# Performance work log

Measured on AMD Instinct MI355X. Metric: run time of the kernel, lower is better.

The kernel has to match this reference:

```python
import jax, jax.numpy as jnp
import numpy as np

PRE_NMS_TOPK = 6000
POST_NMS_TOPK = 1000
NMS_THRESH = 0.7
MIN_SIZE = 16.0
NEG = -1e9  # stand-in for -inf that is safe under autodiff


def setup_inputs() -> dict:
    key = jax.random.key(0)
    k1, k2, k3, k4, k5, k6, k7, k8 = jax.random.split(key, 8)
    B, A = 8, 200000
    N = B * A
    # realistic anchors: centers within a ~1333x800 canvas, sizes 16..256
    cx = jax.random.uniform(k1, (N,), minval=0.0, maxval=1200.0)
    cy = jax.random.uniform(k2, (N,), minval=0.0, maxval=800.0)
    w = jax.random.uniform(k3, (N,), minval=16.0, maxval=256.0)
    h = jax.random.uniform(k4, (N,), minval=16.0, maxval=256.0)
    anchors = jnp.stack([cx - 0.5 * w, cy - 0.5 * h, cx + 0.5 * w, cy + 0.5 * h], axis=1)
    batch_indices = jnp.sort(jax.random.randint(k5, (N,), 0, B)).astype(jnp.int32)
    image_sizes = jax.random.randint(k6, (B, 2), 600, 1334).astype(jnp.int32)  # (H, W)
    objectness_logits = jax.random.normal(k7, (N, 1), dtype=jnp.float32)
    bbox_deltas = jax.random.normal(k8, (N, 4), dtype=jnp.float32) * 0.2
    return {
        'anchors': anchors,
        'batch_indices': batch_indices,
        'image_sizes': image_sizes,
        'objectness_logits': objectness_logits,
        'bbox_deltas': bbox_deltas,
    }


def _nms_one(bx, sc):
    """Greedy NMS on [K,4] boxes / [K] scores; returns POST_NMS_TOPK (idx, ok)."""
    K = bx.shape[0]
    areas = (bx[:, 2] - bx[:, 0]) * (bx[:, 3] - bx[:, 1])
    ar = jnp.arange(K)

    def step(sup, _):
        s = jnp.where(sup, NEG, sc)
        j = jnp.argmax(s)
        ok = s[j] > 0.5 * NEG
        b = bx[j]
        ix1 = jnp.maximum(b[0], bx[:, 0])
        iy1 = jnp.maximum(b[1], bx[:, 1])
        ix2 = jnp.minimum(b[2], bx[:, 2])
        iy2 = jnp.minimum(b[3], bx[:, 3])
        inter = jnp.maximum(ix2 - ix1, 0.0) * jnp.maximum(iy2 - iy1, 0.0)
        iou = inter / (areas + areas[j] - inter + 1e-9)
        sup = sup | (iou > NMS_THRESH) | (ar == j)
        return sup, (j, ok)

    sup0 = sc <= 0.5 * NEG  # padded / invalid entries start suppressed
    _, (idx, ok) = jax.lax.scan(step, sup0, None, length=POST_NMS_TOPK)
    return idx, ok


def reference(anchors, batch_indices, image_sizes, objectness_logits, bbox_deltas):
    B = image_sizes.shape[0]
    N = anchors.shape[0]
    sizes = image_sizes[batch_indices].astype(jnp.float32)  # [N,2] (H,W) per anchor

    # --- box decode ---
    a_w = anchors[:, 2] - anchors[:, 0]
    a_h = anchors[:, 3] - anchors[:, 1]
    a_x = anchors[:, 0] + 0.5 * a_w
    a_y = anchors[:, 1] + 0.5 * a_h
    t_x, t_y = bbox_deltas[:, 0], bbox_deltas[:, 1]
    t_w, t_h = bbox_deltas[:, 2], bbox_deltas[:, 3]
    p_x = a_x + t_x * a_w
    p_y = a_y + t_y * a_h
    p_w = a_w * jnp.exp(jnp.clip(t_w, -10.0, 10.0))
    p_h = a_h * jnp.exp(jnp.clip(t_h, -10.0, 10.0))
    x1 = p_x - 0.5 * p_w
    y1 = p_y - 0.5 * p_h
    x2 = p_x + 0.5 * p_w
    y2 = p_y + 0.5 * p_h

    # --- clip to image ---
    H, W = sizes[:, 0], sizes[:, 1]
    x1 = jnp.clip(x1, 0.0, W - 1.0)
    y1 = jnp.clip(y1, 0.0, H - 1.0)
    x2 = jnp.clip(x2, 0.0, W - 1.0)
    y2 = jnp.clip(y2, 0.0, H - 1.0)
    boxes = jnp.stack([x1, y1, x2, y2], axis=1)  # [N,4]

    # --- min-size filter (as score masking) ---
    valid = ((x2 - x1) >= MIN_SIZE) & ((y2 - y1) >= MIN_SIZE)
    fg = jax.nn.sigmoid(objectness_logits[:, 0])

    # --- per-image top-k over masked scores ---
    img_mask = batch_indices[None, :] == jnp.arange(B, dtype=batch_indices.dtype)[:, None]  # [B,N]
    scores = jnp.where(img_mask & valid[None, :], fg[None, :], NEG)  # [B,N]
    top_scores, top_idx = jax.lax.top_k(scores, PRE_NMS_TOPK)  # [B,PRE]
    top_boxes = boxes[top_idx]  # [B,PRE,4]

    # --- NMS per image ---
    keep_idx, keep_ok = jax.vmap(_nms_one)(top_boxes, top_scores)  # [B,POST]

    sel = jnp.take_along_axis(top_idx, keep_idx, axis=1)  # global anchor indices [B,POST]
    okf = keep_ok[..., None].astype(boxes.dtype)
    props = jnp.take_along_axis(top_boxes, keep_idx[..., None], axis=1) * okf  # [B,POST,4]
    obj = objectness_logits[sel] * okf  # [B,POST,1]
    deltas_out = bbox_deltas[sel] * okf  # [B,POST,4]
    bidx = jnp.where(keep_ok, jnp.arange(B, dtype=jnp.int32)[:, None], -1)  # [B,POST]

    return (props.reshape(-1, 4), bidx.reshape(-1), obj.reshape(-1, 1),
            deltas_out.reshape(-1, 4), keep_ok.reshape(-1))
```

## Files before the change

### kernel.cpp

```cpp
#include <hip/hip_runtime.h>
#include <stdint.h>

#define PRE_K   6000
#define POST_K  1000
#define CAP     8192
#define BINS    1024
#define ROWS    6016
#define CH      94
#define JSPLIT  8
#define NEGF    -1000000000.0f
#define IOU_EPS 16.0f
#define KREG    12


__device__ __forceinline__ uint32_t orderf(float f) {
  uint32_t u = __float_as_uint(f);
  return (u & 0x80000000u) ? ~u : (u | 0x80000000u);
}

__device__ __forceinline__ int score_bin(float sc) {
  int bin = (int)floorf((sc + 12.0f) * ((float)BINS / 24.0f));
  return bin < 0 ? 0 : (bin > BINS - 1 ? BINS - 1 : bin);
}

__device__ __forceinline__ int bin_slot(int bin) {
  return ((bin & 15) << 6) | (bin >> 4);
}

__device__ __forceinline__ void decode_box(
    const float* __restrict__ anchors, const float* __restrict__ deltas,
    const int* __restrict__ isz, int n, int b,
    double& x1, double& y1, double& x2, double& y2, bool& valid) {
  double ax1 = (double)anchors[4 * n + 0], ay1 = (double)anchors[4 * n + 1];
  double ax2 = (double)anchors[4 * n + 2], ay2 = (double)anchors[4 * n + 3];
  double aw = ax2 - ax1, ah = ay2 - ay1;
  double acx = ax1 + 0.5 * aw, acy = ay1 + 0.5 * ah;
  double tx = (double)deltas[4 * n + 0], ty = (double)deltas[4 * n + 1];
  double tw = (double)deltas[4 * n + 2], th = (double)deltas[4 * n + 3];
  tw = tw < -10.0 ? -10.0 : (tw > 10.0 ? 10.0 : tw);
  th = th < -10.0 ? -10.0 : (th > 10.0 ? 10.0 : th);
  double px = acx + tx * aw, py = acy + ty * ah;
  double pw = aw * exp(tw), ph = ah * exp(th);
  double H = (double)isz[2 * b + 0], W = (double)isz[2 * b + 1];
  double wm = W - 1.0, hm = H - 1.0;
  x1 = px - 0.5 * pw; y1 = py - 0.5 * ph;
  x2 = px + 0.5 * pw; y2 = py + 0.5 * ph;
  x1 = fmin(fmax(x1, 0.0), wm); x2 = fmin(fmax(x2, 0.0), wm);
  y1 = fmin(fmax(y1, 0.0), hm); y2 = fmin(fmax(y2, 0.0), hm);
  valid = (x2 - x1 >= 16.0) && (y2 - y1 >= 16.0);
}

__device__ __forceinline__ bool iou_exact(const double* __restrict__ tbox,
                                          const double* __restrict__ tarea,
                                          size_t ri, size_t ci) {
  const double* pr = &tbox[ri * 4];
  const double* pc = &tbox[ci * 4];
  double w = fmin(pr[2], pc[2]) - fmax(pr[0], pc[0]); w = w > 0.0 ? w : 0.0;
  double h = fmin(pr[3], pc[3]) - fmax(pr[1], pc[1]); h = h > 0.0 ? h : 0.0;
  double it = w * h;
  return it > 0.7 * (tarea[ri] + tarea[ci] - it + 1e-9);
}


__global__ void __launch_bounds__(256) k_score(const float* __restrict__ anchors,
                                               const int* __restrict__ bix,
                                               const int* __restrict__ isz,
                                               const float* __restrict__ logits,
                                               const float* __restrict__ deltas,
                                               float* __restrict__ scores,
                                               uint32_t* __restrict__ hist, int N) {
  const int SPAN = 4096;
  int start = blockIdx.x * SPAN;
  int end = start + SPAN < N ? start + SPAN : N;
  __shared__ uint32_t lh[2][BINS];
  for (int i = threadIdx.x; i < 2 * BINS; i += 256) ((uint32_t*)lh)[i] = 0u;
  __shared__ int s_b0, s_b1;
  if (threadIdx.x == 0) { s_b0 = bix[start]; s_b1 = bix[end - 1]; }
  __syncthreads();
  int b0 = s_b0, b1 = s_b1;

  for (int n = start + (int)threadIdx.x; n < end; n += 256) {
    int b = bix[n];
    double x1, y1, x2, y2; bool valid;
    decode_box(anchors, deltas, isz, n, b, x1, y1, x2, y2, valid);
    float sc = valid ? logits[n] : NEGF;
    scores[n] = sc;
    if (valid) {
      int bin = score_bin(sc);
      if (b == b0)      atomicAdd(&lh[0][bin], 1u);
      else if (b == b1) atomicAdd(&lh[1][bin], 1u);
      else              atomicAdd(&hist[b * BINS + bin_slot(bin)], 1u);
    }
  }
  __syncthreads();
  for (int bin = threadIdx.x; bin < BINS; bin += 256) {
    uint32_t c0 = lh[0][bin];
    if (c0) atomicAdd(&hist[b0 * BINS + bin_slot(bin)], c0);
    if (b1 != b0) {
      uint32_t c1 = lh[1][bin];
      if (c1) atomicAdd(&hist[b1 * BINS + bin_slot(bin)], c1);
    }
  }
}

__global__ void __launch_bounds__(1024) k_compact(const float* __restrict__ scores,
                                                  const int* __restrict__ bix,
                                                  const uint32_t* __restrict__ hist,
                                                  uint32_t* __restrict__ cnt,
                                                  uint64_t* __restrict__ cand, int N) {
  const int SPAN = 8192;
  int start = blockIdx.x * SPAN;
  int end = start + SPAN < N ? start + SPAN : N;
  int t = threadIdx.x;
  __shared__ int s_b0, s_b1;
  __shared__ uint32_t sh[BINS];
  __shared__ int s_bs;
  __shared__ uint32_t lcnt[8], lbase[8];
  if (t == 0) { s_b0 = bix[start]; s_b1 = bix[end - 1]; }
  if (t < 8) lcnt[t] = 0u;
  __syncthreads();
  int b0 = s_b0, b1 = s_b1;

  uint32_t bs0 = 0, bs1 = 0;
  for (int pass = 0; pass < 2; pass++) {
    int b = pass == 0 ? b0 : b1;
    if (pass == 1 && b1 == b0) { bs1 = bs0; break; }
    if (t < BINS) sh[t] = hist[b * BINS + bin_slot(t)];
    if (t == 0) s_bs = 0;
    __syncthreads();
    for (int off = 1; off < BINS; off <<= 1) {
      uint32_t v = (t < BINS && t + off < BINS) ? sh[t + off] : 0u;
      __syncthreads();
      if (t < BINS) sh[t] += v;
      __syncthreads();
    }
    if (t < BINS && sh[t] >= PRE_K) atomicMax(&s_bs, t);
    __syncthreads();
    if (pass == 0) bs0 = (uint32_t)s_bs; else bs1 = (uint32_t)s_bs;
    __syncthreads();
  }

  bool     predv[8];
  uint64_t keyv[8];
  uint32_t lposv[8];
  int      bv[8];
  int nt = 0;
  for (int base = start; base < end; base += 1024, nt++) {
    int n = base + t;
    bool pred = false; int b = 0; uint64_t key = 0ull; uint32_t lp = 0u;
    if (n < end) {
      float sc = scores[n];
      if (sc > 0.5f * NEGF) {
        b = bix[n];
        uint32_t bs = (b == b0) ? bs0 : bs1;
        if ((uint32_t)score_bin(sc) >= bs) {
          pred = true;
          key = ((uint64_t)orderf(sc) << 32) | (uint64_t)(uint32_t)(~(uint32_t)n);
          lp = atomicAdd(&lcnt[b], 1u);
        }
      }
    }
    predv[nt] = pred; keyv[nt] = key; lposv[nt] = lp; bv[nt] = b;
  }
  __syncthreads();
  if (t < 8) {
    uint32_t c = lcnt[t];
    lbase[t] = c ? atomicAdd(&cnt[t], c) : 0u;
  }
  __syncthreads();
  for (int k = 0; k < nt; k++) {
    if (predv[k]) {
      uint32_t pos = lbase[bv[k]] + lposv[k];
      if (pos < CAP) cand[(size_t)bv[k] * CAP + pos] = keyv[k];
    }
  }
}

__global__ void __launch_bounds__(256) k_rank(const uint64_t* __restrict__ cand,
                                              const uint32_t* __restrict__ cnt,
                                              uint32_t* __restrict__ prank) {
  int blk = blockIdx.x;
  int js = blk % JSPLIT;
  int ic = (blk / JSPLIT) % 32;
  int b  = blk / (JSPLIT * 32);
  int t = threadIdx.x;
  int C = (int)min(cnt[b], (uint32_t)CAP);
  if (ic * 256 >= C) return;
  const uint64_t* g = cand + (size_t)b * CAP;
  int i = ic * 256 + t;
  uint64_t ki = (i < C) ? g[i] : 0ull;

  int q = (C + JSPLIT - 1) / JSPLIT;
  int j0 = js * q;
  int j1 = j0 + q < C ? j0 + q : C;

  __shared__ uint64_t tile[1024];
  int rank = 0;
  for (int base = j0; base < j1; base += 1024) {
#pragma unroll
    for (int u = 0; u < 4; u++) {
      int j = base + u * 256 + t;
      tile[u * 256 + t] = (j < j1) ? g[j] : 0ull;
    }
    __syncthreads();
    int lim = j1 - base < 1024 ? j1 - base : 1024;
    const ulonglong2* t2 = (const ulonglong2*)tile;
    int pairs = lim >> 1;
    int jj = 0;
    for (; jj + 4 <= pairs; jj += 4) {
      ulonglong2 v0 = t2[jj + 0], v1 = t2[jj + 1];
      ulonglong2 v2 = t2[jj + 2], v3 = t2[jj + 3];
      rank += (v0.x > ki) ? 1 : 0; rank += (v0.y > ki) ? 1 : 0;
      rank += (v1.x > ki) ? 1 : 0; rank += (v1.y > ki) ? 1 : 0;
      rank += (v2.x > ki) ? 1 : 0; rank += (v2.y > ki) ? 1 : 0;
      rank += (v3.x > ki) ? 1 : 0; rank += (v3.y > ki) ? 1 : 0;
    }
    for (; jj < pairs; jj++) {
      ulonglong2 v = t2[jj];
      rank += (v.x > ki) ? 1 : 0; rank += (v.y > ki) ? 1 : 0;
    }
    if (lim & 1) rank += (tile[lim - 1] > ki) ? 1 : 0;
    __syncthreads();
  }
  if (i < C) prank[((size_t)b * JSPLIT + js) * CAP + i] = (uint32_t)rank;
}

__global__ void __launch_bounds__(256) k_place_gather(
    const uint64_t* __restrict__ cand, const uint32_t* __restrict__ cnt,
    const uint32_t* __restrict__ prank,
    const float* __restrict__ anchors, const float* __restrict__ deltas,
    const int* __restrict__ isz,
    double* __restrict__ tbox, double* __restrict__ tarea,
    float4* __restrict__ tboxf, float* __restrict__ tareaf,
    int* __restrict__ top_n, int* __restrict__ Cnum, int B) {
  int idx = blockIdx.x * blockDim.x + threadIdx.x;
  if (idx >= B * CAP) return;
  int b = idx / CAP, i = idx % CAP;
  int C = (int)min(cnt[b], (uint32_t)CAP);
  if (i == 0) Cnum[b] = C < PRE_K ? C : PRE_K;
  if (i >= C) return;
  uint32_t rank = 0;
#pragma unroll
  for (int js = 0; js < JSPLIT; js++)
    rank += prank[((size_t)b * JSPLIT + js) * CAP + i];
  if (rank >= PRE_K) return;
  int n = (int)(~(uint32_t)(cand[idx] & 0xFFFFFFFFull));
  double x1, y1, x2, y2; bool valid;
  decode_box(anchors, deltas, isz, n, b, x1, y1, x2, y2, valid);
  size_t row = (size_t)b * ROWS + rank;
  tbox[row * 4 + 0] = x1;
  tbox[row * 4 + 1] = y1;
  tbox[row * 4 + 2] = x2;
  tbox[row * 4 + 3] = y2;
  double ar = (x2 - x1) * (y2 - y1);
  tarea[row] = ar;
  tboxf[row] = make_float4((float)x1, (float)y1, (float)x2, (float)y2);
  tareaf[row] = (float)ar;
  top_n[b * PRE_K + rank] = n;
}

__global__ void __launch_bounds__(64) k_iou_mat(const float4* __restrict__ tboxf,
                                                const float* __restrict__ tareaf,
                                                const double* __restrict__ tbox,
                                                const double* __restrict__ tarea,
                                                const int* __restrict__ Cnum,
                                                uint32_t* __restrict__ maskT) {
  int rc = blockIdx.x;
  int cc = blockIdx.y;
  int b  = blockIdx.z;
  if (rc > cc) return;
  int C = Cnum[b];
  if (cc * 64 >= C) return;
  int lane = threadIdx.x;
  size_t bb = (size_t)b * ROWS;

  float4 rb4 = tboxf[bb + (size_t)rc * 64 + lane];
  float  sra = 0.7f * tareaf[bb + (size_t)rc * 64 + lane];
  __shared__ float4 cbx[64];
  __shared__ float  csa[64];
  cbx[lane] = tboxf[bb + (size_t)cc * 64 + lane];
  csa[lane] = 0.7f * tareaf[bb + (size_t)cc * 64 + lane];
  __syncthreads();

  bool isdiag = (rc == cc);
  uint32_t res0 = 0u, res1 = 0u;

  for (int j = 0; j < 64; j++) {
    float4 c4 = cbx[j];
    float sca = csa[j];
    float iw = fminf(c4.z, rb4.z) - fmaxf(c4.x, rb4.x);
    float ih = fminf(c4.w, rb4.w) - fmaxf(c4.y, rb4.y);
    iw = fmaxf(iw, 0.0f); ih = fmaxf(ih, 0.0f);
    float inter = iw * ih;
    float diff = fmaf(1.7f, inter, -(sra + sca));
    bool gt = isdiag ? (j > lane) : true;
    bool sup = gt && (diff > IOU_EPS);
    if (gt && !sup && diff > -IOU_EPS) {
      sup = iou_exact(tbox, tarea, bb + (size_t)rc * 64 + lane,
                      bb + (size_t)cc * 64 + j);
    }
    if (sup) { if (j < 32) res0 |= 1u << j; else res1 |= 1u << (j & 31); }
  }
  uint2* seg = (uint2*)(maskT + (((size_t)b * CH + cc) * ROWS + (size_t)rc * 64) * 2);
  seg[lane] = make_uint2(res0, res1);
}

__global__ void __launch_bounds__(256) k_nms_reduce(const uint32_t* __restrict__ maskT,
                                                    const double* __restrict__ tbox,
                                                    const int* __restrict__ Cnum,
                                                    const int* __restrict__ top_n,
                                                    const float* __restrict__ logits,
                                                    const float* __restrict__ deltas,
                                                    float* __restrict__ out, int B) {
  int b = blockIdx.x, t = threadIdx.x;
  int wave = t >> 6, lane = t & 63;
  int C = Cnum[b];
  int nch = (C + 63) >> 6;
  const uint32_t* Mb = maskT + (size_t)b * CH * ROWS * 2;
  size_t bb = (size_t)b * ROWS;

  __shared__ uint32_t acc[CH][2];
  __shared__ uint16_t kept[POST_K];
  __shared__ uint16_t pend[2][64];
  __shared__ int      npend[2];
  __shared__ uint64_t s_kept;

  for (int i = t; i < CH * 2; i += 256) ((uint32_t*)acc)[i] = 0u;
  if (t < 2) npend[t] = 0;
  __syncthreads();

  uint2 dgv = make_uint2(0u, 0u), pfv = make_uint2(0u, 0u), pfv2 = make_uint2(0u, 0u);
  if (wave == 0 && nch > 0) {
    dgv = *(const uint2*)(Mb + ((size_t)0 * ROWS + lane) * 2);
    if (nch > 1) pfv  = *(const uint2*)(Mb + ((size_t)1 * ROWS + lane) * 2);
    if (nch > 2) pfv2 = *(const uint2*)(Mb + ((size_t)2 * ROWS + lane) * 2);
  }

  uint2 lz[KREG];
#pragma unroll
  for (int u = 0; u < KREG; u++) lz[u] = make_uint2(0u, 0u);
  int lz_total = 0, lz_cc0 = 0, lz_span = 1;

  int nkept = 0;
  for (int c = 0; c < nch; c++) {
    if (wave == 0) {
      int base = c << 6;
      uint64_t sup = (uint64_t)acc[c][0] | ((uint64_t)acc[c][1] << 32);
      int rem = C - base;
      if (rem < 64) sup |= ~((1ull << rem) - 1ull);
      uint64_t diag = (uint64_t)dgv.x | ((uint64_t)dgv.y << 32);
      uint64_t keptMask = 0ull;
      uint64_t alive = ~sup;
      uint64_t m = alive;
      while (m) {
        int i = __builtin_ctzll(m);
        keptMask |= 1ull << i;
        uint64_t d = (uint64_t)__shfl((long long)diag, i, 64);
        sup |= d | (1ull << i);
        m = alive & ~sup;
      }
      int allowed = POST_K - nkept;
      int pc2 = __popcll(keptMask);
      while (pc2 > allowed) {
        keptMask &= ~(1ull << (63 - __builtin_clzll(keptMask)));
        pc2--;
      }
      if (lane == 0) { s_kept = keptMask; npend[c & 1] = pc2; }
      bool mine = (keptMask >> lane) & 1ull;
      if (mine) {
        int pfx = __popcll(keptMask & ((1ull << lane) - 1ull));
        kept[nkept + pfx] = (uint16_t)(base + lane);
        pend[c & 1][pfx] = (uint16_t)(base + lane);
      }
      if (c + 1 < nch) {
        uint32_t v0 = mine ? pfv.x : 0u, v1 = mine ? pfv.y : 0u;
        uint32_t w0 = mine ? pfv2.x : 0u, w1 = mine ? pfv2.y : 0u;
#pragma unroll
        for (int off = 32; off > 0; off >>= 1) {
          v0 |= (uint32_t)__shfl_xor((int)v0, off, 64);
          v1 |= (uint32_t)__shfl_xor((int)v1, off, 64);
          w0 |= (uint32_t)__shfl_xor((int)w0, off, 64);
          w1 |= (uint32_t)__shfl_xor((int)w1, off, 64);
        }
        if (lane == 0) {
          if (v0) atomicOr(&acc[c + 1][0], v0);
          if (v1) atomicOr(&acc[c + 1][1], v1);
          if (c + 2 < nch) {
            if (w0) atomicOr(&acc[c + 2][0], w0);
            if (w1) atomicOr(&acc[c + 2][1], w1);
          }
        }
        int nb = base + 64;
        dgv = *(const uint2*)(Mb + (((size_t)(c + 1)) * ROWS + nb + lane) * 2);
        if (c + 2 < nch) pfv  = *(const uint2*)(Mb + (((size_t)(c + 2)) * ROWS + nb + lane) * 2);
        else             pfv  = make_uint2(0u, 0u);
        if (c + 3 < nch) pfv2 = *(const uint2*)(Mb + (((size_t)(c + 3)) * ROWS + nb + lane) * 2);
        else             pfv2 = make_uint2(0u, 0u);
      }
    } else {
      if (lz_total > 0) {
#pragma unroll
        for (int u = 0; u < KREG; u++) {
          int it = (t - 64) + u * 192;
          if (it < lz_total) {
            int pi = it / lz_span;
            int cc = lz_cc0 + (it - pi * lz_span);
            if (lz[u].x) atomicOr(&acc[cc][0], lz[u].x);
            if (lz[u].y) atomicOr(&acc[cc][1], lz[u].y);
          }
        }
      }
      int np = (c >= 1) ? npend[(c - 1) & 1] : 0;
      int cc0 = c + 2;
      int span = nch - cc0;
      if (np > 0 && span > 0) {
        int total = np * span;
#pragma unroll
        for (int u = 0; u < KREG; u++) {
          int it = (t - 64) + u * 192;
          uint2 v = make_uint2(0u, 0u);
          if (it < total) {
            int pi = it / span;
            int cc = cc0 + (it - pi * span);
            int row = (int)pend[(c - 1) & 1][pi];
            v = *(const uint2*)(Mb + ((size_t)cc * ROWS + row) * 2);
          }
          lz[u] = v;
        }
        for (int it = (t - 64) + KREG * 192; it < total; it += 192) {
          int pi = it / span;
          int cc = cc0 + (it - pi * span);
          int row = (int)pend[(c - 1) & 1][pi];
          uint2 v = *(const uint2*)(Mb + ((size_t)cc * ROWS + row) * 2);
          if (v.x) atomicOr(&acc[cc][0], v.x);
          if (v.y) atomicOr(&acc[cc][1], v.y);
        }
        lz_total = total < KREG * 192 ? total : KREG * 192;
        lz_cc0 = cc0; lz_span = span;
      } else {
        lz_total = 0;
      }
    }
    __syncthreads();

    int pc = __popcll(s_kept);
    nkept += pc;
    if (nkept >= POST_K) break;
  }

  __syncthreads();
  int M_out = B * POST_K;
  for (int s2 = t; s2 < POST_K; s2 += 256) {
    float p0 = 0.f, p1 = 0.f, p2 = 0.f, p3 = 0.f;
    float ob = 0.f, d0f = 0.f, d1f = 0.f, d2f = 0.f, d3f = 0.f;
    float bi = -1.0f, okv = 0.0f;
    if (s2 < nkept) {
      int j = (int)kept[s2];
      int n = top_n[b * PRE_K + j];
      const double* p = &tbox[(bb + j) * 4];
      p0 = (float)p[0]; p1 = (float)p[1]; p2 = (float)p[2]; p3 = (float)p[3];
      ob = logits[n];
      d0f = deltas[4 * n + 0]; d1f = deltas[4 * n + 1];
      d2f = deltas[4 * n + 2]; d3f = deltas[4 * n + 3];
      bi = (float)b; okv = 1.0f;
    }
    int idx = b * POST_K + s2;
    out[idx * 4 + 0] = p0;
    out[idx * 4 + 1] = p1;
    out[idx * 4 + 2] = p2;
    out[idx * 4 + 3] = p3;
    out[4 * M_out + idx] = bi;
    out[5 * M_out + idx] = ob;
    out[6 * M_out + idx * 4 + 0] = d0f;
    out[6 * M_out + idx * 4 + 1] = d1f;
    out[6 * M_out + idx * 4 + 2] = d2f;
    out[6 * M_out + idx * 4 + 3] = d3f;
    out[10 * M_out + idx] = okv;
  }
}


extern "C" void kernel_launch(void* const* d_in, const int* in_sizes, int n_in,
                              void* d_out, int out_size, void* d_ws, size_t ws_size,
                              hipStream_t stream) {
  const float* anchors = (const float*)d_in[0];
  const int*   bix     = (const int*)d_in[1];
  const int*   isz     = (const int*)d_in[2];
  const float* logits  = (const float*)d_in[3];
  const float* deltas  = (const float*)d_in[4];
  float* out = (float*)d_out;

  int N = in_sizes[1];
  int B = in_sizes[2] / 2;

  uintptr_t p = (uintptr_t)d_ws;
  double*   tbox   = (double*)p;    p += (size_t)B * ROWS * 4 * sizeof(double);
  double*   tarea  = (double*)p;    p += (size_t)B * ROWS * sizeof(double);
  uint64_t* cand   = (uint64_t*)p;  p += (size_t)B * CAP * sizeof(uint64_t);
  float*    scores = (float*)p;     p += (size_t)N * sizeof(float);
  uint32_t* hist   = (uint32_t*)p;  p += (size_t)B * BINS * sizeof(uint32_t);
  uint32_t* cnt    = (uint32_t*)p;  p += (size_t)B * sizeof(uint32_t);
  uint32_t* prank  = (uint32_t*)p;  p += (size_t)B * JSPLIT * CAP * sizeof(uint32_t);
  int*      top_n    = (int*)p;     p += (size_t)B * PRE_K * sizeof(int);
  int*      Cnum     = (int*)p;      p += (size_t)B * sizeof(int);
  p = (p + 255) & ~(uintptr_t)255;
  uint32_t* maskT    = (uint32_t*)p; p += (size_t)B * CH * ROWS * 2 * sizeof(uint32_t);
  float4*   tboxf  = (float4*)scores;
  float*    tareaf = (float*)(scores + (size_t)B * ROWS * 4);
  (void)ws_size; (void)n_in; (void)out_size;

  hipMemsetAsync(hist, 0, (size_t)(B * BINS + B) * sizeof(uint32_t), stream);
  k_score<<<(N + 4095) / 4096, 256, 0, stream>>>(anchors, bix, isz, logits, deltas,
                                                 scores, hist, N);
  k_compact<<<(N + 8191) / 8192, 1024, 0, stream>>>(scores, bix, hist, cnt, cand, N);
  k_rank<<<B * 32 * JSPLIT, 256, 0, stream>>>(cand, cnt, prank);
  k_place_gather<<<(B * CAP + 255) / 256, 256, 0, stream>>>(cand, cnt, prank,
                                                            anchors, deltas, isz,
                                                            tbox, tarea, tboxf,
                                                            tareaf, top_n, Cnum, B);
  dim3 iou_grid(CH, CH, B);
  k_iou_mat<<<iou_grid, 64, 0, stream>>>(tboxf, tareaf, tbox, tarea, Cnum, maskT);
  k_nms_reduce<<<B, 256, 0, stream>>>(maskT, tbox, Cnum, top_n, logits, deltas,
                                      out, B);
}
```

Baseline: 385.4 us.

## Fuse rank and placement kernels, restructure IoU mask layout into band and row-major

Merges the split rank kernel and the placement/gather kernel into one kernel that computes full ranks per candidate and directly decodes and places boxes, removing the partial-rank buffer and one launch. The IoU mask kernel now processes 8 column chunks per block and writes near-diagonal chunks to a compact band buffer and far chunks to a row-major buffer. The NMS reduce reads the band buffer with double-buffered prefetch and gathers far rows contiguously per row. The aim is fewer launches and more coalesced mask access, at the cost of less parallelism in ranking and more work per IoU block.

```diff
diff --git a/kernel.cpp b/kernel.cpp
--- a/kernel.cpp
+++ b/kernel.cpp
@@ -7,7 +7,7 @@
 #define BINS    1024
 #define ROWS    6016
 #define CH      94
-#define JSPLIT  8
+#define CHP     96
 #define NEGF    -1000000000.0f
 #define IOU_EPS 16.0f
 #define KREG    12
@@ -176,34 +176,33 @@
   }
 }
 
-__global__ void __launch_bounds__(256) k_rank(const uint64_t* __restrict__ cand,
-                                              const uint32_t* __restrict__ cnt,
-                                              uint32_t* __restrict__ prank) {
-  int blk = blockIdx.x;
-  int js = blk % JSPLIT;
-  int ic = (blk / JSPLIT) % 32;
-  int b  = blk / (JSPLIT * 32);
+__global__ void __launch_bounds__(256) k_rank_place(
+    const uint64_t* __restrict__ cand, const uint32_t* __restrict__ cnt,
+    const float* __restrict__ anchors, const float* __restrict__ deltas,
+    const int* __restrict__ isz,
+    double* __restrict__ tbox, double* __restrict__ tarea,
+    float4* __restrict__ tboxf, float* __restrict__ tareaf,
+    int* __restrict__ top_n, int* __restrict__ Cnum, int B) {
+  int ic = blockIdx.x & 31;
+  int b  = blockIdx.x >> 5;
   int t = threadIdx.x;
   int C = (int)min(cnt[b], (uint32_t)CAP);
+  if (ic == 0 && t == 0) Cnum[b] = C < PRE_K ? C : PRE_K;
   if (ic * 256 >= C) return;
   const uint64_t* g = cand + (size_t)b * CAP;
   int i = ic * 256 + t;
   uint64_t ki = (i < C) ? g[i] : 0ull;
 
-  int q = (C + JSPLIT - 1) / JSPLIT;
-  int j0 = js * q;
-  int j1 = j0 + q < C ? j0 + q : C;
-
   __shared__ uint64_t tile[1024];
   int rank = 0;
-  for (int base = j0; base < j1; base += 1024) {
+  for (int base = 0; base < C; base += 1024) {
 #pragma unroll
     for (int u = 0; u < 4; u++) {
       int j = base + u * 256 + t;
-      tile[u * 256 + t] = (j < j1) ? g[j] : 0ull;
-    }
-    __syncthreads();
-    int lim = j1 - base < 1024 ? j1 - base : 1024;
+      tile[u * 256 + t] = (j < C) ? g[j] : 0ull;
+    }
+    __syncthreads();
+    int lim = C - base < 1024 ? C - base : 1024;
     const ulonglong2* t2 = (const ulonglong2*)tile;
     int pairs = lim >> 1;
     int jj = 0;
@@ -222,29 +221,9 @@
     if (lim & 1) rank += (tile[lim - 1] > ki) ? 1 : 0;
     __syncthreads();
   }
-  if (i < C) prank[((size_t)b * JSPLIT + js) * CAP + i] = (uint32_t)rank;
-}
-
-__global__ void __launch_bounds__(256) k_place_gather(
-    const uint64_t* __restrict__ cand, const uint32_t* __restrict__ cnt,
-    const uint32_t* __restrict__ prank,
-    const float* __restrict__ anchors, const float* __restrict__ deltas,
-    const int* __restrict__ isz,
-    double* __restrict__ tbox, double* __restrict__ tarea,
-    float4* __restrict__ tboxf, float* __restrict__ tareaf,
-    int* __restrict__ top_n, int* __restrict__ Cnum, int B) {
-  int idx = blockIdx.x * blockDim.x + threadIdx.x;
-  if (idx >= B * CAP) return;
-  int b = idx / CAP, i = idx % CAP;
-  int C = (int)min(cnt[b], (uint32_t)CAP);
-  if (i == 0) Cnum[b] = C < PRE_K ? C : PRE_K;
-  if (i >= C) return;
-  uint32_t rank = 0;
-#pragma unroll
-  for (int js = 0; js < JSPLIT; js++)
-    rank += prank[((size_t)b * JSPLIT + js) * CAP + i];
-  if (rank >= PRE_K) return;
-  int n = (int)(~(uint32_t)(cand[idx] & 0xFFFFFFFFull));
+  if (i >= C || rank >= PRE_K) return;
+
+  int n = (int)(~(uint32_t)(ki & 0xFFFFFFFFull));
   double x1, y1, x2, y2; bool valid;
   decode_box(anchors, deltas, isz, n, b, x1, y1, x2, y2, valid);
   size_t row = (size_t)b * ROWS + rank;
@@ -264,13 +243,17 @@
                                                 const double* __restrict__ tbox,
                                                 const double* __restrict__ tarea,
                                                 const int* __restrict__ Cnum,
-                                                uint32_t* __restrict__ maskT) {
-  int rc = blockIdx.x;
-  int cc = blockIdx.y;
+                                                uint32_t* __restrict__ maskB,
+                                                uint32_t* __restrict__ maskR) {
+  int g  = blockIdx.x;
+  int rc = blockIdx.y;
   int b  = blockIdx.z;
-  if (rc > cc) return;
   int C = Cnum[b];
-  if (cc * 64 >= C) return;
+  int nch = (C + 63) >> 6;
+  if (rc >= nch) return;
+  int cc_lo = g << 3;
+  int cc_hi = (cc_lo + 8 < nch) ? cc_lo + 8 : nch;
+  if (cc_lo >= nch || cc_hi <= rc) return;
   int lane = threadIdx.x;
   size_t bb = (size_t)b * ROWS;
 
@@ -278,34 +261,59 @@
   float  sra = 0.7f * tareaf[bb + (size_t)rc * 64 + lane];
   __shared__ float4 cbx[64];
   __shared__ float  csa[64];
-  cbx[lane] = tboxf[bb + (size_t)cc * 64 + lane];
-  csa[lane] = 0.7f * tareaf[bb + (size_t)cc * 64 + lane];
-  __syncthreads();
-
-  bool isdiag = (rc == cc);
-  uint32_t res0 = 0u, res1 = 0u;
-
-  for (int j = 0; j < 64; j++) {
-    float4 c4 = cbx[j];
-    float sca = csa[j];
-    float iw = fminf(c4.z, rb4.z) - fmaxf(c4.x, rb4.x);
-    float ih = fminf(c4.w, rb4.w) - fmaxf(c4.y, rb4.y);
-    iw = fmaxf(iw, 0.0f); ih = fmaxf(ih, 0.0f);
-    float inter = iw * ih;
-    float diff = fmaf(1.7f, inter, -(sra + sca));
-    bool gt = isdiag ? (j > lane) : true;
-    bool sup = gt && (diff > IOU_EPS);
-    if (gt && !sup && diff > -IOU_EPS) {
-      sup = iou_exact(tbox, tarea, bb + (size_t)rc * 64 + lane,
-                      bb + (size_t)cc * 64 + j);
-    }
-    if (sup) { if (j < 32) res0 |= 1u << j; else res1 |= 1u << (j & 31); }
-  }
-  uint2* seg = (uint2*)(maskT + (((size_t)b * CH + cc) * ROWS + (size_t)rc * 64) * 2);
-  seg[lane] = make_uint2(res0, res1);
-}
-
-__global__ void __launch_bounds__(256) k_nms_reduce(const uint32_t* __restrict__ maskT,
+
+  uint2 fr[8];
+#pragma unroll
+  for (int u = 0; u < 8; u++) fr[u] = make_uint2(0u, 0u);
+  bool any_far = false;
+
+#pragma unroll
+  for (int u = 0; u < 8; u++) {
+    int cc = cc_lo + u;
+    if (cc < rc || cc >= cc_hi) continue;
+    __syncthreads();
+    cbx[lane] = tboxf[bb + (size_t)cc * 64 + lane];
+    csa[lane] = 0.7f * tareaf[bb + (size_t)cc * 64 + lane];
+    __syncthreads();
+    int d = cc - rc;
+    bool isdiag = (d == 0);
+    uint32_t r0 = 0u, r1 = 0u;
+    for (int j = 0; j < 64; j++) {
+      float4 c4 = cbx[j];
+      float sca = csa[j];
+      float iw = fminf(c4.z, rb4.z) - fmaxf(c4.x, rb4.x);
+      float ih = fminf(c4.w, rb4.w) - fmaxf(c4.y, rb4.y);
+      iw = fmaxf(iw, 0.0f); ih = fmaxf(ih, 0.0f);
+      float inter = iw * ih;
+      float diff = fmaf(1.7f, inter, -(sra + sca));
+      bool gt = isdiag ? (j > lane) : true;
+      bool sup = gt && (diff > IOU_EPS);
+      if (gt && !sup && diff > -IOU_EPS) {
+        sup = iou_exact(tbox, tarea, bb + (size_t)rc * 64 + lane,
+                        bb + (size_t)cc * 64 + j);
+      }
+      if (sup) { if (j < 32) r0 |= 1u << j; else r1 |= 1u << (j & 31); }
+    }
+    if (d <= 2) {
+      uint2* bp = (uint2*)maskB + (((size_t)b * CH + rc) * 3 + d) * 64;
+      bp[lane] = make_uint2(r0, r1);
+    } else {
+      fr[u] = make_uint2(r0, r1);
+      any_far = true;
+    }
+  }
+  if (any_far) {
+    size_t base = (bb + (size_t)rc * 64 + lane) * CHP + cc_lo;
+    uint4* dst = (uint4*)(maskR + base * 2);
+    dst[0] = make_uint4(fr[0].x, fr[0].y, fr[1].x, fr[1].y);
+    dst[1] = make_uint4(fr[2].x, fr[2].y, fr[3].x, fr[3].y);
+    dst[2] = make_uint4(fr[4].x, fr[4].y, fr[5].x, fr[5].y);
+    dst[3] = make_uint4(fr[6].x, fr[6].y, fr[7].x, fr[7].y);
+  }
+}
+
+__global__ void __launch_bounds__(256) k_nms_reduce(const uint32_t* __restrict__ maskB,
+                                                    const uint32_t* __restrict__ maskR,
                                                     const double* __restrict__ tbox,
                                                     const int* __restrict__ Cnum,
                                                     const int* __restrict__ top_n,
@@ -316,7 +324,8 @@
   int wave = t >> 6, lane = t & 63;
   int C = Cnum[b];
   int nch = (C + 63) >> 6;
-  const uint32_t* Mb = maskT + (size_t)b * CH * ROWS * 2;
+  const uint2* Bb = (const uint2*)maskB + (size_t)b * CH * 3 * 64;
+  const uint2* Rb = (const uint2*)maskR + (size_t)b * ROWS * CHP;
   size_t bb = (size_t)b * ROWS;
 
   __shared__ uint32_t acc[CH][2];
@@ -329,11 +338,19 @@
   if (t < 2) npend[t] = 0;
   __syncthreads();
 
-  uint2 dgv = make_uint2(0u, 0u), pfv = make_uint2(0u, 0u), pfv2 = make_uint2(0u, 0u);
-  if (wave == 0 && nch > 0) {
-    dgv = *(const uint2*)(Mb + ((size_t)0 * ROWS + lane) * 2);
-    if (nch > 1) pfv  = *(const uint2*)(Mb + ((size_t)1 * ROWS + lane) * 2);
-    if (nch > 2) pfv2 = *(const uint2*)(Mb + ((size_t)2 * ROWS + lane) * 2);
+  uint2 dgA = make_uint2(0u,0u), pfA = make_uint2(0u,0u), qfA = make_uint2(0u,0u);
+  uint2 dgB = make_uint2(0u,0u), pfB = make_uint2(0u,0u), qfB = make_uint2(0u,0u);
+  if (wave == 0) {
+    if (nch > 0) {
+      dgA = Bb[((size_t)0 * 3 + 0) * 64 + lane];
+      pfA = Bb[((size_t)0 * 3 + 1) * 64 + lane];
+      qfA = Bb[((size_t)0 * 3 + 2) * 64 + lane];
+    }
+    if (nch > 1) {
+      dgB = Bb[((size_t)1 * 3 + 0) * 64 + lane];
+      pfB = Bb[((size_t)1 * 3 + 1) * 64 + lane];
+      qfB = Bb[((size_t)1 * 3 + 2) * 64 + lane];
+    }
   }
 
   uint2 lz[KREG];
@@ -344,6 +361,9 @@
   int nkept = 0;
   for (int c = 0; c < nch; c++) {
     if (wave == 0) {
+      uint2 dgv, pfv, qfv;
+      if (c & 1) { dgv = dgB; pfv = pfB; qfv = qfB; }
+      else       { dgv = dgA; pfv = pfA; qfv = qfA; }
       int base = c << 6;
       uint64_t sup = (uint64_t)acc[c][0] | ((uint64_t)acc[c][1] << 32);
       int rem = C - base;
@@ -374,7 +394,7 @@
       }
       if (c + 1 < nch) {
         uint32_t v0 = mine ? pfv.x : 0u, v1 = mine ? pfv.y : 0u;
-        uint32_t w0 = mine ? pfv2.x : 0u, w1 = mine ? pfv2.y : 0u;
+        uint32_t w0 = mine ? qfv.x : 0u, w1 = mine ? qfv.y : 0u;
 #pragma unroll
         for (int off = 32; off > 0; off >>= 1) {
           v0 |= (uint32_t)__shfl_xor((int)v0, off, 64);
@@ -390,12 +410,17 @@
             if (w1) atomicOr(&acc[c + 2][1], w1);
           }
         }
-        int nb = base + 64;
-        dgv = *(const uint2*)(Mb + (((size_t)(c + 1)) * ROWS + nb + lane) * 2);
-        if (c + 2 < nch) pfv  = *(const uint2*)(Mb + (((size_t)(c + 2)) * ROWS + nb + lane) * 2);
-        else             pfv  = make_uint2(0u, 0u);
-        if (c + 3 < nch) pfv2 = *(const uint2*)(Mb + (((size_t)(c + 3)) * ROWS + nb + lane) * 2);
-        else             pfv2 = make_uint2(0u, 0u);
+      }
+      if (c + 2 < nch) {
+        if (c & 1) {
+          dgB = Bb[((size_t)(c + 2) * 3 + 0) * 64 + lane];
+          pfB = Bb[((size_t)(c + 2) * 3 + 1) * 64 + lane];
+          qfB = Bb[((size_t)(c + 2) * 3 + 2) * 64 + lane];
+        } else {
+          dgA = Bb[((size_t)(c + 2) * 3 + 0) * 64 + lane];
+          pfA = Bb[((size_t)(c + 2) * 3 + 1) * 64 + lane];
+          qfA = Bb[((size_t)(c + 2) * 3 + 2) * 64 + lane];
+        }
       }
     } else {
       if (lz_total > 0) {
@@ -423,7 +448,7 @@
             int pi = it / span;
             int cc = cc0 + (it - pi * span);
             int row = (int)pend[(c - 1) & 1][pi];
-            v = *(const uint2*)(Mb + ((size_t)cc * ROWS + row) * 2);
+            v = Rb[(size_t)row * CHP + cc];
           }
           lz[u] = v;
         }
@@ -431,7 +456,7 @@
           int pi = it / span;
           int cc = cc0 + (it - pi * span);
           int row = (int)pend[(c - 1) & 1][pi];
-          uint2 v = *(const uint2*)(Mb + ((size_t)cc * ROWS + row) * 2);
+          uint2 v = Rb[(size_t)row * CHP + cc];
           if (v.x) atomicOr(&acc[cc][0], v.x);
           if (v.y) atomicOr(&acc[cc][1], v.y);
         }
@@ -500,11 +525,12 @@
   float*    scores = (float*)p;     p += (size_t)N * sizeof(float);
   uint32_t* hist   = (uint32_t*)p;  p += (size_t)B * BINS * sizeof(uint32_t);
   uint32_t* cnt    = (uint32_t*)p;  p += (size_t)B * sizeof(uint32_t);
-  uint32_t* prank  = (uint32_t*)p;  p += (size_t)B * JSPLIT * CAP * sizeof(uint32_t);
-  int*      top_n    = (int*)p;     p += (size_t)B * PRE_K * sizeof(int);
-  int*      Cnum     = (int*)p;      p += (size_t)B * sizeof(int);
+  int*      top_n  = (int*)p;       p += (size_t)B * PRE_K * sizeof(int);
+  int*      Cnum   = (int*)p;       p += (size_t)B * sizeof(int);
   p = (p + 255) & ~(uintptr_t)255;
-  uint32_t* maskT    = (uint32_t*)p; p += (size_t)B * CH * ROWS * 2 * sizeof(uint32_t);
+  uint32_t* maskB  = (uint32_t*)p;  p += (size_t)B * CH * 3 * 64 * 2 * sizeof(uint32_t);
+  p = (p + 255) & ~(uintptr_t)255;
+  uint32_t* maskR  = (uint32_t*)p;  p += (size_t)B * ROWS * CHP * 2 * sizeof(uint32_t);
   float4*   tboxf  = (float4*)scores;
   float*    tareaf = (float*)(scores + (size_t)B * ROWS * 4);
   (void)ws_size; (void)n_in; (void)out_size;
@@ -513,13 +539,12 @@
   k_score<<<(N + 4095) / 4096, 256, 0, stream>>>(anchors, bix, isz, logits, deltas,
                                                  scores, hist, N);
   k_compact<<<(N + 8191) / 8192, 1024, 0, stream>>>(scores, bix, hist, cnt, cand, N);
-  k_rank<<<B * 32 * JSPLIT, 256, 0, stream>>>(cand, cnt, prank);
-  k_place_gather<<<(B * CAP + 255) / 256, 256, 0, stream>>>(cand, cnt, prank,
-                                                            anchors, deltas, isz,
-                                                            tbox, tarea, tboxf,
-                                                            tareaf, top_n, Cnum, B);
-  dim3 iou_grid(CH, CH, B);
-  k_iou_mat<<<iou_grid, 64, 0, stream>>>(tboxf, tareaf, tbox, tarea, Cnum, maskT);
-  k_nms_reduce<<<B, 256, 0, stream>>>(maskT, tbox, Cnum, top_n, logits, deltas,
-                                      out, B);
-}
+  k_rank_place<<<B * 32, 256, 0, stream>>>(cand, cnt, anchors, deltas, isz,
+                                           tbox, tarea, tboxf, tareaf,
+                                           top_n, Cnum, B);
+  dim3 iou_grid(12, CH, B);
+  k_iou_mat<<<iou_grid, 64, 0, stream>>>(tboxf, tareaf, tbox, tarea, Cnum,
+                                         maskB, maskR);
+  k_nms_reduce<<<B, 256, 0, stream>>>(maskB, maskR, tbox, Cnum, top_n,
+                                      logits, deltas, out, B);
+}
```

Measured after the change: 512.5 us. 33.0% more time.
